# Performance work log

Hardware: AMD Instinct MI355X
Metric: run time of the kernel (lower is better)

## Reference

```python
import jax, jax.numpy as jnp
import numpy as np

DT = 0.01  # RK45 step size ts


def setup_inputs() -> dict:
    key = jax.random.key(0)
    ks = jax.random.split(key, 8)
    B, T, NU, NX, NH, NY = 512, 256, 64, 128, 1024, 16
    scale = 0.05  # keep dynamics stable under explicit integration
    return {
        "u": jax.random.normal(ks[0], (B, T, NU), jnp.float32),
        "x0": jax.random.normal(ks[1], (B, NX), jnp.float32),
        "W1": jax.random.normal(ks[2], (NH, NX + NU), jnp.float32) * scale,
        "b1": jnp.zeros((NH,), jnp.float32),
        "W2": jax.random.normal(ks[3], (NX, NH), jnp.float32) * scale,
        "b2": jnp.zeros((NX,), jnp.float32),
        "C": jax.random.normal(ks[4], (NY, NX), jnp.float32) * scale,
        "D": jax.random.normal(ks[5], (NY, NU), jnp.float32) * scale,
    }


def reference(u, x0, W1, b1, W2, b2, C, D):
    dt = jnp.asarray(DT, u.dtype)

    def ss_model(u_t, x):
        # nonlinear state-space model: dx = W2 tanh(W1 [x;u] + b1) + b2, y = Cx + Du
        z = jnp.concatenate([x, u_t], axis=-1)              # [B, nx+nu]
        k = jnp.tanh(z @ W1.T + b1) @ W2.T + b2             # [B, nx]
        y = x @ C.T + u_t @ D.T                             # [B, ny]
        return k, y

    def step(x, u_t):
        k1, y = ss_model(u_t, x)
        k2, _ = ss_model(u_t, x + dt / 4 * k1)
        k3, _ = ss_model(u_t, x + dt / 32 * (3 * k1 + 9 * k2))
        k4, _ = ss_model(u_t, x + dt / 2197 * (1932 * k1 - 7200 * k2 + 7296 * k3))
        k5, _ = ss_model(u_t, x + dt * (439 * k1 / 216 - 8 * k2 + 3680 * k3 / 513 - 845 * k4 / 4104))
        k6, _ = ss_model(u_t, x + dt * (-8 * k1 / 27 + 2 * k2 - 3544 * k3 / 2565 + 1859 * k4 / 4104 - 11 * k5 / 40))
        dx = dt * (16 * k1 / 135 + 6656 * k3 / 12825 + 28561 * k4 / 56430 - 9 * k5 / 50 + 2 * k6 / 55)
        return x + dx, (x, y)

    u_t_first = jnp.swapaxes(u, 0, 1)                        # [T, B, nu]
    _, (X, Y) = jax.lax.scan(step, x0, u_t_first)
    X_sim = jnp.swapaxes(X, 0, 1)                            # [B, T, nx]
    Y_sim = jnp.swapaxes(Y, 0, 1)                            # [B, T, ny]
    return X_sim, Y_sim
```

## Files before the change

### kernel.cpp

```cpp
#include <hip/hip_runtime.h>

typedef short bf16x8 __attribute__((ext_vector_type(8)));
typedef float f32x4 __attribute__((ext_vector_type(4)));

static constexpr int kT  = 256;
static constexpr int kNU = 64;
static constexpr int kNX = 128;
static constexpr int kNY = 16;
static constexpr int kBT = 16;

static constexpr int kW1P = 64 * 6 * 64 * 8;
static constexpr int kW2P = 8 * 32 * 64 * 8;
static constexpr int kCP  = 4 * 64 * 8;
static constexpr int kDP  = 2 * 64 * 8;
static constexpr int kPackTotal = kW1P + kW2P + kCP + kDP;

__device__ __forceinline__ unsigned short f2bf(float f) {
  union { float f; unsigned int u; } v; v.f = f;
  unsigned int r = v.u + 0x7fffu + ((v.u >> 16) & 1u);
  return (unsigned short)(r >> 16);
}

__global__ __launch_bounds__(256)
void prepack_kernel(const float* __restrict__ W1, const float* __restrict__ W2,
                    const float* __restrict__ C, const float* __restrict__ D,
                    unsigned short* __restrict__ wp) {
  int i = blockIdx.x * 256 + threadIdx.x;
  if (i >= kPackTotal) return;
  float v;
  if (i < kW1P) {
    int j = i & 7, l = (i >> 3) & 63, t = i >> 9;
    int ks = t % 6, n = t / 6;
    v = W1[(16 * n + (l & 15)) * 192 + 32 * ks + 8 * (l >> 4) + j];
  } else if (i < kW1P + kW2P) {
    int k = i - kW1P;
    int j = k & 7, l = (k >> 3) & 63, t = k >> 9;
    int ks = t & 31, n = t >> 5;
    v = W2[(16 * n + (l & 15)) * 1024 + 32 * ks + 8 * (l >> 4) + j];
  } else if (i < kW1P + kW2P + kCP) {
    int k = i - (kW1P + kW2P);
    int j = k & 7, l = (k >> 3) & 63, ks = k >> 9;
    v = C[(l & 15) * 128 + 32 * ks + 8 * (l >> 4) + j];
  } else {
    int k = i - (kW1P + kW2P + kCP);
    int j = k & 7, l = (k >> 3) & 63, ks = k >> 9;
    v = D[(l & 15) * 64 + 32 * ks + 8 * (l >> 4) + j];
  }
  wp[i] = f2bf(v);
}

__constant__ float CTc[5][5] = {
  {(float)(0.01 / 4.0), 0.f, 0.f, 0.f, 0.f},
  {(float)(0.01 * 3.0 / 32.0), (float)(0.01 * 9.0 / 32.0), 0.f, 0.f, 0.f},
  {(float)(0.01 * 1932.0 / 2197.0), (float)(-0.01 * 7200.0 / 2197.0), (float)(0.01 * 7296.0 / 2197.0), 0.f, 0.f},
  {(float)(0.01 * 439.0 / 216.0), (float)(-0.01 * 8.0), (float)(0.01 * 3680.0 / 513.0), (float)(-0.01 * 845.0 / 4104.0), 0.f},
  {(float)(-0.01 * 8.0 / 27.0), (float)(0.01 * 2.0), (float)(-0.01 * 3544.0 / 2565.0), (float)(0.01 * 1859.0 / 4104.0), (float)(-0.01 * 11.0 / 40.0)}
};

__device__ __forceinline__ float tanh_fast(float x) {
  float t = exp2f(x * 2.8853900817779268f);
  return 1.0f - 2.0f * __builtin_amdgcn_rcpf(t + 1.0f);
}

__device__ __forceinline__ void gll16(const void* g, void* l) {
  __builtin_amdgcn_global_load_lds((const __attribute__((address_space(1))) unsigned int*)g,
                                   (__attribute__((address_space(3))) unsigned int*)l, 16, 0, 0);
}

#define MFMA_BF16(A, B, C) __builtin_amdgcn_mfma_f32_16x16x32_bf16(A, B, C, 0, 0, 0)
#define VM_WAIT4 asm volatile("s_waitcnt vmcnt(4)" ::: "memory")
#define BARRIER_LGKM do { asm volatile("s_waitcnt lgkmcnt(0)" ::: "memory"); \
                          __builtin_amdgcn_s_barrier(); } while (0)

#define ISSUE_FRAG(P_) do {                                                    \
    int _p = (P_) & 63;                                                        \
    const char* _src;                                                          \
    if (_p < 32) _src = wpb + (((8 * w + (_p >> 2)) * 6 + (_p & 3)) << 10) + lane * 16; \
    else         _src = wpb + ((size_t)kW1P * 2) + ((w * 32 + (_p - 32)) << 10) + lane * 16; \
    gll16(_src, &wbuf[_p & 7][w][0]);                                          \
  } while (0)

#define READ4(V0_, V1_, V2_, V3_, B_) do {                                     \
    VM_WAIT4;                                                                  \
    V0_ = *(const bf16x8*)&wbuf[((B_) + 0) & 7][w][lane * 8];                  \
    V1_ = *(const bf16x8*)&wbuf[((B_) + 1) & 7][w][lane * 8];                  \
    V2_ = *(const bf16x8*)&wbuf[((B_) + 2) & 7][w][lane * 8];                  \
    V3_ = *(const bf16x8*)&wbuf[((B_) + 3) & 7][w][lane * 8];                  \
  } while (0)

#define REFILL4(B_) do {                                                       \
    __builtin_amdgcn_sched_barrier(0);                                         \
    ISSUE_FRAG((B_) + 8); ISSUE_FRAG((B_) + 9);                                \
    ISSUE_FRAG((B_) + 10); ISSUE_FRAG((B_) + 11);                              \
  } while (0)

__global__ __launch_bounds__(512, 2)
void rk45_kernel(const float* __restrict__ u, const float* __restrict__ x0,
                 const float* __restrict__ b1g, const float* __restrict__ b2g,
                 const unsigned short* __restrict__ wp,
                 float* __restrict__ Xout, float* __restrict__ Yout) {
  __shared__ __align__(16) unsigned short zs[16][232];
  __shared__ __align__(16) unsigned short hs[16][1048];
  __shared__ __align__(16) float xs[16][132];
  __shared__ __align__(16) unsigned short wbuf[8][8][512];

  const int tid  = threadIdx.x;
  const int lane = tid & 63;
  const int w    = tid >> 6;
  const int r16  = lane & 15;
  const int g    = lane >> 4;
  const int b0   = blockIdx.x * kBT;
  const int colw = 16 * w + r16;

  const char* wpb = (const char*)wp;
  const bf16x8* W1P = (const bf16x8*)wp;
  const bf16x8* CP  = (const bf16x8*)(wp + kW1P + kW2P);
  const bf16x8* DP  = (const bf16x8*)(wp + kW1P + kW2P + kCP);

  float b1r[8];
  #pragma unroll
  for (int nt = 0; nt < 8; ++nt)
    b1r[nt] = b1g[128 * w + 16 * nt + r16];
  const float b2reg = b2g[colw];

  float xreg[4];
  f32x4 ubias[8];
  f32x4 k1r = {0,0,0,0}, k2r = {0,0,0,0}, k3r = {0,0,0,0}, k4r = {0,0,0,0}, k5r = {0,0,0,0};

  #pragma unroll
  for (int q = 0; q < 4; ++q) {
    int row = 4 * g + q;
    float xv = x0[(b0 + row) * kNX + colw];
    xreg[q] = xv;
    xs[row][colw] = xv;
    zs[row][colw] = f2bf(xv);
  }

  const int urow = tid >> 5, ucol = (tid & 31) * 2;
  float2 ureg = *(const float2*)&u[((b0 + urow) * kT + 0) * kNU + ucol];

  #pragma unroll
  for (int p = 0; p < 8; ++p) ISSUE_FRAG(p);
  __syncthreads();

  const float D1 = (float)(0.01 * 16.0 / 135.0);
  const float D3 = (float)(0.01 * 6656.0 / 12825.0);
  const float D4 = (float)(0.01 * 28561.0 / 56430.0);
  const float D5 = (float)(-0.01 * 9.0 / 50.0);
  const float D6 = (float)(0.01 * 2.0 / 55.0);

  #pragma unroll 1
  for (int t = 0; t < kT; ++t) {
    {
      int base = tid * 4, row = base >> 7, col = base & 127;
      float4 xv = *(const float4*)&xs[row][col];
      *(float4*)&Xout[((b0 + row) * kT + t) * kNX + col] = xv;
      zs[urow][kNX + ucol]     = f2bf(ureg.x);
      zs[urow][kNX + ucol + 1] = f2bf(ureg.y);
      if (t + 1 < kT)
        ureg = *(const float2*)&u[((b0 + urow) * kT + (t + 1)) * kNU + ucol];
    }
    BARRIER_LGKM;

    {
      bf16x8 zu0 = *(const bf16x8*)&zs[r16][8 * g + 128];
      bf16x8 zu1 = *(const bf16x8*)&zs[r16][8 * g + 160];
      #pragma unroll
      for (int nt = 0; nt < 8; ++nt) {
        int n = 8 * w + nt;
        bf16x8 uw0 = W1P[(n * 6 + 4) * 64 + lane];
        bf16x8 uw1 = W1P[(n * 6 + 5) * 64 + lane];
        float bv = b1r[nt];
        f32x4 ua = {bv, bv, bv, bv};
        ua = MFMA_BF16(zu0, uw0, ua);
        ua = MFMA_BF16(zu1, uw1, ua);
        ubias[nt] = ua;
      }
    }

    #pragma unroll 1
    for (int e = 0; e < 6; ++e) {
      bf16x8 za0 = *(const bf16x8*)&zs[r16][8 * g + 0];
      bf16x8 za1 = *(const bf16x8*)&zs[r16][8 * g + 32];
      bf16x8 za2 = *(const bf16x8*)&zs[r16][8 * g + 64];
      bf16x8 za3 = *(const bf16x8*)&zs[r16][8 * g + 96];

      #pragma unroll
      for (int nt = 0; nt < 8; ++nt) {
        bf16x8 fr0, fr1, fr2, fr3;
        READ4(fr0, fr1, fr2, fr3, 4 * nt);

        f32x4 aa = {0,0,0,0}, ab = {0,0,0,0};
        aa = MFMA_BF16(za0, fr0, aa);
        ab = MFMA_BF16(za1, fr1, ab);
        aa = MFMA_BF16(za2, fr2, aa);
        ab = MFMA_BF16(za3, fr3, ab);
        REFILL4(4 * nt);

        int n = 8 * w + nt;
        #pragma unroll
        for (int q = 0; q < 4; ++q) {
          float hv = tanh_fast(aa[q] + ab[q] + ubias[nt][q]);
          hs[4 * g + q][16 * n + r16] = f2bf(hv);
        }
      }

      if (e == 0 && w == 0) {
        bf16x8 zu0 = *(const bf16x8*)&zs[r16][8 * g + 128];
        bf16x8 zu1 = *(const bf16x8*)&zs[r16][8 * g + 160];
        f32x4 ay = {0,0,0,0};
        ay = MFMA_BF16(za0, CP[0 * 64 + lane], ay);
        ay = MFMA_BF16(za1, CP[1 * 64 + lane], ay);
        ay = MFMA_BF16(za2, CP[2 * 64 + lane], ay);
        ay = MFMA_BF16(za3, CP[3 * 64 + lane], ay);
        ay = MFMA_BF16(zu0, DP[lane], ay);
        ay = MFMA_BF16(zu1, DP[64 + lane], ay);
        #pragma unroll
        for (int q = 0; q < 4; ++q)
          Yout[((b0 + 4 * g + q) * kT + t) * kNY + r16] = ay[q];
      }
      BARRIER_LGKM;

      f32x4 ka = {0,0,0,0}, kb = {0,0,0,0};
      #pragma unroll
      for (int j = 0; j < 8; ++j) {
        bf16x8 g0, g1, g2, g3;
        READ4(g0, g1, g2, g3, 32 + 4 * j);

        bf16x8 h0 = *(const bf16x8*)&hs[r16][8 * g + 32 * (4 * j + 0)];
        bf16x8 h1 = *(const bf16x8*)&hs[r16][8 * g + 32 * (4 * j + 1)];
        bf16x8 h2 = *(const bf16x8*)&hs[r16][8 * g + 32 * (4 * j + 2)];
        bf16x8 h3 = *(const bf16x8*)&hs[r16][8 * g + 32 * (4 * j + 3)];
        ka = MFMA_BF16(h0, g0, ka);
        kb = MFMA_BF16(h1, g1, kb);
        ka = MFMA_BF16(h2, g2, ka);
        kb = MFMA_BF16(h3, g3, kb);
        REFILL4(32 + 4 * j);
      }
      f32x4 kv = ka + kb;
      #pragma unroll
      for (int q = 0; q < 4; ++q) kv[q] += b2reg;

      if      (e == 0) k1r = kv;
      else if (e == 1) k2r = kv;
      else if (e == 2) k3r = kv;
      else if (e == 3) k4r = kv;
      else if (e == 4) k5r = kv;

      if (e < 5) {
        float c1 = CTc[e][0], c2 = CTc[e][1], c3 = CTc[e][2], c4 = CTc[e][3], c5 = CTc[e][4];
        #pragma unroll
        for (int q = 0; q < 4; ++q) {
          float xt = xreg[q] + c1 * k1r[q] + c2 * k2r[q] + c3 * k3r[q] + c4 * k4r[q] + c5 * k5r[q];
          zs[4 * g + q][colw] = f2bf(xt);
        }
      } else {
        #pragma unroll
        for (int q = 0; q < 4; ++q) {
          float xn = xreg[q] + (D1 * k1r[q] + D3 * k3r[q] + D4 * k4r[q] + D5 * k5r[q] + D6 * kv[q]);
          xreg[q] = xn;
          xs[4 * g + q][colw] = xn;
          zs[4 * g + q][colw] = f2bf(xn);
        }
      }
      BARRIER_LGKM;
    }
  }
}

extern "C" void kernel_launch(void* const* d_in, const int* in_sizes, int n_in,
                              void* d_out, int out_size, void* d_ws, size_t ws_size,
                              hipStream_t stream) {
  const float* u  = (const float*)d_in[0];
  const float* x0 = (const float*)d_in[1];
  const float* W1 = (const float*)d_in[2];
  const float* b1 = (const float*)d_in[3];
  const float* W2 = (const float*)d_in[4];
  const float* b2 = (const float*)d_in[5];
  const float* C  = (const float*)d_in[6];
  const float* D  = (const float*)d_in[7];

  unsigned short* wp = (unsigned short*)d_ws;
  float* Xout = (float*)d_out;
  float* Yout = Xout + (size_t)512 * 256 * 128;

  hipLaunchKernelGGL(prepack_kernel, dim3((kPackTotal + 255) / 256), dim3(256), 0, stream,
                     W1, W2, C, D, wp);
  hipLaunchKernelGGL(rk45_kernel, dim3(32), dim3(512), 0, stream,
                     u, x0, b1, b2, (const unsigned short*)wp, Xout, Yout);
}
```

Before: 10.70 ms.

## Stream weight fragments through register ring instead of LDS global_load_lds buffer

Replaces the LDS staging buffer filled by global_load_lds with an 8-entry register ring of bf16x8 fragments. The ring is loaded directly from global memory, with vmcnt waits pacing the prefetch across the W1-u, W1-x and W2 phases. The C/D weights are now staged once in LDS instead of being read from global memory each step, and launch bounds drop to one block per SM so the kernel has room for the extra registers. This removes the LDS round-trip for weights, but relies on manual vmcnt counting being exact. Halving occupancy may also expose global-load latency.

```diff
diff --git a/kernel.cpp b/kernel.cpp
--- a/kernel.cpp
+++ b/kernel.cpp
@@ -62,39 +62,12 @@
   return 1.0f - 2.0f * __builtin_amdgcn_rcpf(t + 1.0f);
 }
 
-__device__ __forceinline__ void gll16(const void* g, void* l) {
-  __builtin_amdgcn_global_load_lds((const __attribute__((address_space(1))) unsigned int*)g,
-                                   (__attribute__((address_space(3))) unsigned int*)l, 16, 0, 0);
-}
-
 #define MFMA_BF16(A, B, C) __builtin_amdgcn_mfma_f32_16x16x32_bf16(A, B, C, 0, 0, 0)
-#define VM_WAIT4 asm volatile("s_waitcnt vmcnt(4)" ::: "memory")
+#define VM_WAIT(N) asm volatile("s_waitcnt vmcnt(" #N ")" ::: "memory")
 #define BARRIER_LGKM do { asm volatile("s_waitcnt lgkmcnt(0)" ::: "memory"); \
                           __builtin_amdgcn_s_barrier(); } while (0)
 
-#define ISSUE_FRAG(P_) do {                                                    \
-    int _p = (P_) & 63;                                                        \
-    const char* _src;                                                          \
-    if (_p < 32) _src = wpb + (((8 * w + (_p >> 2)) * 6 + (_p & 3)) << 10) + lane * 16; \
-    else         _src = wpb + ((size_t)kW1P * 2) + ((w * 32 + (_p - 32)) << 10) + lane * 16; \
-    gll16(_src, &wbuf[_p & 7][w][0]);                                          \
-  } while (0)
-
-#define READ4(V0_, V1_, V2_, V3_, B_) do {                                     \
-    VM_WAIT4;                                                                  \
-    V0_ = *(const bf16x8*)&wbuf[((B_) + 0) & 7][w][lane * 8];                  \
-    V1_ = *(const bf16x8*)&wbuf[((B_) + 1) & 7][w][lane * 8];                  \
-    V2_ = *(const bf16x8*)&wbuf[((B_) + 2) & 7][w][lane * 8];                  \
-    V3_ = *(const bf16x8*)&wbuf[((B_) + 3) & 7][w][lane * 8];                  \
-  } while (0)
-
-#define REFILL4(B_) do {                                                       \
-    __builtin_amdgcn_sched_barrier(0);                                         \
-    ISSUE_FRAG((B_) + 8); ISSUE_FRAG((B_) + 9);                                \
-    ISSUE_FRAG((B_) + 10); ISSUE_FRAG((B_) + 11);                              \
-  } while (0)
-
-__global__ __launch_bounds__(512, 2)
+__global__ __launch_bounds__(512, 1)
 void rk45_kernel(const float* __restrict__ u, const float* __restrict__ x0,
                  const float* __restrict__ b1g, const float* __restrict__ b2g,
                  const unsigned short* __restrict__ wp,
@@ -102,7 +75,7 @@
   __shared__ __align__(16) unsigned short zs[16][232];
   __shared__ __align__(16) unsigned short hs[16][1048];
   __shared__ __align__(16) float xs[16][132];
-  __shared__ __align__(16) unsigned short wbuf[8][8][512];
+  __shared__ __align__(16) unsigned short cdl[384][8];
 
   const int tid  = threadIdx.x;
   const int lane = tid & 63;
@@ -112,10 +85,15 @@
   const int b0   = blockIdx.x * kBT;
   const int colw = 16 * w + r16;
 
-  const char* wpb = (const char*)wp;
   const bf16x8* W1P = (const bf16x8*)wp;
-  const bf16x8* CP  = (const bf16x8*)(wp + kW1P + kW2P);
-  const bf16x8* DP  = (const bf16x8*)(wp + kW1P + kW2P + kCP);
+  const bf16x8* W2P = (const bf16x8*)(wp + kW1P);
+
+#define W1XF(NT, KS) W1P[((8 * w + (NT)) * 6 + (KS)) * 64 + lane]
+#define W1UF(NT, J)  W1P[((8 * w + (NT)) * 6 + 4 + (J)) * 64 + lane]
+#define W2F(IDX)     W2P[(w * 32 + (IDX)) * 64 + lane]
+
+  if (tid < 384)
+    *(bf16x8*)&cdl[tid][0] = ((const bf16x8*)(wp + kW1P + kW2P))[tid];
 
   float b1r[8];
   #pragma unroll
@@ -139,8 +117,10 @@
   const int urow = tid >> 5, ucol = (tid & 31) * 2;
   float2 ureg = *(const float2*)&u[((b0 + urow) * kT + 0) * kNU + ucol];
 
+  bf16x8 ring[8];
   #pragma unroll
-  for (int p = 0; p < 8; ++p) ISSUE_FRAG(p);
+  for (int s = 0; s < 8; ++s)
+    ring[s] = W1UF(s >> 1, s & 1);
   __syncthreads();
 
   const float D1 = (float)(0.01 * 16.0 / 135.0);
@@ -167,9 +147,16 @@
       bf16x8 zu1 = *(const bf16x8*)&zs[r16][8 * g + 160];
       #pragma unroll
       for (int nt = 0; nt < 8; ++nt) {
-        int n = 8 * w + nt;
-        bf16x8 uw0 = W1P[(n * 6 + 4) * 64 + lane];
-        bf16x8 uw1 = W1P[(n * 6 + 5) * 64 + lane];
+        VM_WAIT(6);
+        bf16x8 uw0 = ring[(2 * nt) & 7];
+        bf16x8 uw1 = ring[(2 * nt + 1) & 7];
+        if (nt < 4) {
+          ring[(2 * nt) & 7]     = W1UF(nt + 4, 0);
+          ring[(2 * nt + 1) & 7] = W1UF(nt + 4, 1);
+        } else {
+          ring[(2 * nt) & 7]     = W1XF((2 * nt - 8) >> 2, (2 * nt - 8) & 3);
+          ring[(2 * nt + 1) & 7] = W1XF((2 * nt - 7) >> 2, (2 * nt - 7) & 3);
+        }
         float bv = b1r[nt];
         f32x4 ua = {bv, bv, bv, bv};
         ua = MFMA_BF16(zu0, uw0, ua);
@@ -187,15 +174,23 @@
 
       #pragma unroll
       for (int nt = 0; nt < 8; ++nt) {
-        bf16x8 fr0, fr1, fr2, fr3;
-        READ4(fr0, fr1, fr2, fr3, 4 * nt);
+        VM_WAIT(4);
+        bf16x8 fr0 = ring[(4 * nt + 0) & 7];
+        bf16x8 fr1 = ring[(4 * nt + 1) & 7];
+        bf16x8 fr2 = ring[(4 * nt + 2) & 7];
+        bf16x8 fr3 = ring[(4 * nt + 3) & 7];
+        #pragma unroll
+        for (int r = 0; r < 4; ++r) {
+          const int qr = 4 * nt + 8 + r;
+          if (qr < 32) ring[(4 * nt + r) & 7] = W1XF(qr >> 2, qr & 3);
+          else         ring[(4 * nt + r) & 7] = W2F(qr - 32);
+        }
 
         f32x4 aa = {0,0,0,0}, ab = {0,0,0,0};
         aa = MFMA_BF16(za0, fr0, aa);
         ab = MFMA_BF16(za1, fr1, ab);
         aa = MFMA_BF16(za2, fr2, aa);
         ab = MFMA_BF16(za3, fr3, ab);
-        REFILL4(4 * nt);
 
         int n = 8 * w + nt;
         #pragma unroll
@@ -209,12 +204,12 @@
         bf16x8 zu0 = *(const bf16x8*)&zs[r16][8 * g + 128];
         bf16x8 zu1 = *(const bf16x8*)&zs[r16][8 * g + 160];
         f32x4 ay = {0,0,0,0};
-        ay = MFMA_BF16(za0, CP[0 * 64 + lane], ay);
-        ay = MFMA_BF16(za1, CP[1 * 64 + lane], ay);
-        ay = MFMA_BF16(za2, CP[2 * 64 + lane], ay);
-        ay = MFMA_BF16(za3, CP[3 * 64 + lane], ay);
-        ay = MFMA_BF16(zu0, DP[lane], ay);
-        ay = MFMA_BF16(zu1, DP[64 + lane], ay);
+        ay = MFMA_BF16(za0, *(const bf16x8*)&cdl[0 * 64 + lane][0], ay);
+        ay = MFMA_BF16(za1, *(const bf16x8*)&cdl[1 * 64 + lane][0], ay);
+        ay = MFMA_BF16(za2, *(const bf16x8*)&cdl[2 * 64 + lane][0], ay);
+        ay = MFMA_BF16(za3, *(const bf16x8*)&cdl[3 * 64 + lane][0], ay);
+        ay = MFMA_BF16(zu0, *(const bf16x8*)&cdl[4 * 64 + lane][0], ay);
+        ay = MFMA_BF16(zu1, *(const bf16x8*)&cdl[5 * 64 + lane][0], ay);
         #pragma unroll
         for (int q = 0; q < 4; ++q)
           Yout[((b0 + 4 * g + q) * kT + t) * kNY + r16] = ay[q];
@@ -224,8 +219,18 @@
       f32x4 ka = {0,0,0,0}, kb = {0,0,0,0};
       #pragma unroll
       for (int j = 0; j < 8; ++j) {
-        bf16x8 g0, g1, g2, g3;
-        READ4(g0, g1, g2, g3, 32 + 4 * j);
+        VM_WAIT(4);
+        bf16x8 g0 = ring[(4 * j + 0) & 7];
+        bf16x8 g1 = ring[(4 * j + 1) & 7];
+        bf16x8 g2 = ring[(4 * j + 2) & 7];
+        bf16x8 g3 = ring[(4 * j + 3) & 7];
+        #pragma unroll
+        for (int r = 0; r < 4; ++r) {
+          const int qr = 40 + 4 * j + r;
+          if (qr < 64)    ring[(4 * j + r) & 7] = W2F(qr - 32);
+          else if (e < 5) ring[(4 * j + r) & 7] = W1XF((qr - 64) >> 2, (qr - 64) & 3);
+          else            ring[(4 * j + r) & 7] = W1UF((qr - 64) >> 1, (qr - 64) & 1);
+        }
 
         bf16x8 h0 = *(const bf16x8*)&hs[r16][8 * g + 32 * (4 * j + 0)];
         bf16x8 h1 = *(const bf16x8*)&hs[r16][8 * g + 32 * (4 * j + 1)];
@@ -235,7 +240,6 @@
         kb = MFMA_BF16(h1, g1, kb);
         ka = MFMA_BF16(h2, g2, ka);
         kb = MFMA_BF16(h3, g3, kb);
-        REFILL4(32 + 4 * j);
       }
       f32x4 kv = ka + kb;
       #pragma unroll
```

Result: slower. 11.08 ms (+3.5%).

## Stream weight fragments into registers with pinned first tiles instead of LDS ring

Applied to the files above, without the earlier changes.

Removes the global_load_lds ring buffer in shared memory that streamed W1/W2 fragments. Weights now load straight into registers through two alternating register sets, with each next fragment prefetched right after the current MFMAs. The first W1 and W2 tiles stay resident in registers for the whole run, so each pass refetches fewer fragments. This drops the LDS round trip and the vmcnt waits, but raises register pressure and relies on L1/L2 latency being hidden by one fragment of lookahead.

```diff
diff --git a/kernel.cpp b/kernel.cpp
--- a/kernel.cpp
+++ b/kernel.cpp
@@ -62,39 +62,11 @@
   return 1.0f - 2.0f * __builtin_amdgcn_rcpf(t + 1.0f);
 }
 
-__device__ __forceinline__ void gll16(const void* g, void* l) {
-  __builtin_amdgcn_global_load_lds((const __attribute__((address_space(1))) unsigned int*)g,
-                                   (__attribute__((address_space(3))) unsigned int*)l, 16, 0, 0);
-}
-
 #define MFMA_BF16(A, B, C) __builtin_amdgcn_mfma_f32_16x16x32_bf16(A, B, C, 0, 0, 0)
-#define VM_WAIT4 asm volatile("s_waitcnt vmcnt(4)" ::: "memory")
 #define BARRIER_LGKM do { asm volatile("s_waitcnt lgkmcnt(0)" ::: "memory"); \
                           __builtin_amdgcn_s_barrier(); } while (0)
 
-#define ISSUE_FRAG(P_) do {                                                    \
-    int _p = (P_) & 63;                                                        \
-    const char* _src;                                                          \
-    if (_p < 32) _src = wpb + (((8 * w + (_p >> 2)) * 6 + (_p & 3)) << 10) + lane * 16; \
-    else         _src = wpb + ((size_t)kW1P * 2) + ((w * 32 + (_p - 32)) << 10) + lane * 16; \
-    gll16(_src, &wbuf[_p & 7][w][0]);                                          \
-  } while (0)
-
-#define READ4(V0_, V1_, V2_, V3_, B_) do {                                     \
-    VM_WAIT4;                                                                  \
-    V0_ = *(const bf16x8*)&wbuf[((B_) + 0) & 7][w][lane * 8];                  \
-    V1_ = *(const bf16x8*)&wbuf[((B_) + 1) & 7][w][lane * 8];                  \
-    V2_ = *(const bf16x8*)&wbuf[((B_) + 2) & 7][w][lane * 8];                  \
-    V3_ = *(const bf16x8*)&wbuf[((B_) + 3) & 7][w][lane * 8];                  \
-  } while (0)
-
-#define REFILL4(B_) do {                                                       \
-    __builtin_amdgcn_sched_barrier(0);                                         \
-    ISSUE_FRAG((B_) + 8); ISSUE_FRAG((B_) + 9);                                \
-    ISSUE_FRAG((B_) + 10); ISSUE_FRAG((B_) + 11);                              \
-  } while (0)
-
-__global__ __launch_bounds__(512, 2)
+__global__ __launch_bounds__(512) __attribute__((amdgpu_waves_per_eu(2, 2)))
 void rk45_kernel(const float* __restrict__ u, const float* __restrict__ x0,
                  const float* __restrict__ b1g, const float* __restrict__ b2g,
                  const unsigned short* __restrict__ wp,
@@ -102,7 +74,6 @@
   __shared__ __align__(16) unsigned short zs[16][232];
   __shared__ __align__(16) unsigned short hs[16][1048];
   __shared__ __align__(16) float xs[16][132];
-  __shared__ __align__(16) unsigned short wbuf[8][8][512];
 
   const int tid  = threadIdx.x;
   const int lane = tid & 63;
@@ -112,10 +83,19 @@
   const int b0   = blockIdx.x * kBT;
   const int colw = 16 * w + r16;
 
-  const char* wpb = (const char*)wp;
   const bf16x8* W1P = (const bf16x8*)wp;
+  const bf16x8* W2P = (const bf16x8*)(wp + kW1P);
   const bf16x8* CP  = (const bf16x8*)(wp + kW1P + kW2P);
   const bf16x8* DP  = (const bf16x8*)(wp + kW1P + kW2P + kCP);
+
+#define LOAD_W1X(F0, F1, F2, F3, NT) do {                          \
+    const bf16x8* _p = W1P + (8 * w + (NT)) * 6 * 64 + lane;       \
+    F0 = _p[0]; F1 = _p[64]; F2 = _p[128]; F3 = _p[192];           \
+  } while (0)
+#define LOAD_W2(F0, F1, F2, F3, CC) do {                           \
+    const bf16x8* _p = W2P + (w * 32 + 4 * (CC)) * 64 + lane;      \
+    F0 = _p[0]; F1 = _p[64]; F2 = _p[128]; F3 = _p[192];           \
+  } while (0)
 
   float b1r[8];
   #pragma unroll
@@ -139,8 +119,14 @@
   const int urow = tid >> 5, ucol = (tid & 31) * 2;
   float2 ureg = *(const float2*)&u[((b0 + urow) * kT + 0) * kNU + ucol];
 
-  #pragma unroll
-  for (int p = 0; p < 8; ++p) ISSUE_FRAG(p);
+  bf16x8 p10, p11, p12, p13;
+  bf16x8 p20, p21, p22, p23;
+  bf16x8 fA0, fA1, fA2, fA3;
+  bf16x8 fB0, fB1, fB2, fB3;
+  LOAD_W1X(p10, p11, p12, p13, 0);
+  LOAD_W2 (p20, p21, p22, p23, 0);
+  LOAD_W1X(fA0, fA1, fA2, fA3, 1);
+  LOAD_W1X(fB0, fB1, fB2, fB3, 2);
   __syncthreads();
 
   const float D1 = (float)(0.01 * 16.0 / 135.0);
@@ -185,25 +171,26 @@
       bf16x8 za2 = *(const bf16x8*)&zs[r16][8 * g + 64];
       bf16x8 za3 = *(const bf16x8*)&zs[r16][8 * g + 96];
 
-      #pragma unroll
-      for (int nt = 0; nt < 8; ++nt) {
-        bf16x8 fr0, fr1, fr2, fr3;
-        READ4(fr0, fr1, fr2, fr3, 4 * nt);
-
-        f32x4 aa = {0,0,0,0}, ab = {0,0,0,0};
-        aa = MFMA_BF16(za0, fr0, aa);
-        ab = MFMA_BF16(za1, fr1, ab);
-        aa = MFMA_BF16(za2, fr2, aa);
-        ab = MFMA_BF16(za3, fr3, ab);
-        REFILL4(4 * nt);
-
-        int n = 8 * w + nt;
-        #pragma unroll
-        for (int q = 0; q < 4; ++q) {
-          float hv = tanh_fast(aa[q] + ab[q] + ubias[nt][q]);
-          hs[4 * g + q][16 * n + r16] = f2bf(hv);
-        }
-      }
+#define MM1(NT, F0, F1, F2, F3, ISS)                                   \
+      { f32x4 aa = {0,0,0,0}, ab = {0,0,0,0};                          \
+        aa = MFMA_BF16(za0, F0, aa); ab = MFMA_BF16(za1, F1, ab);      \
+        aa = MFMA_BF16(za2, F2, aa); ab = MFMA_BF16(za3, F3, ab);      \
+        ISS;                                                           \
+        int n = 8 * w + (NT);                                          \
+        _Pragma("unroll")                                              \
+        for (int q = 0; q < 4; ++q) {                                  \
+          float hv = tanh_fast(aa[q] + ab[q] + ubias[NT][q]);          \
+          hs[4 * g + q][16 * n + r16] = f2bf(hv);                      \
+        } }
+      MM1(0, p10, p11, p12, p13, {});
+      MM1(1, fA0, fA1, fA2, fA3, LOAD_W1X(fA0, fA1, fA2, fA3, 3));
+      MM1(2, fB0, fB1, fB2, fB3, LOAD_W1X(fB0, fB1, fB2, fB3, 4));
+      MM1(3, fA0, fA1, fA2, fA3, LOAD_W1X(fA0, fA1, fA2, fA3, 5));
+      MM1(4, fB0, fB1, fB2, fB3, LOAD_W1X(fB0, fB1, fB2, fB3, 6));
+      MM1(5, fA0, fA1, fA2, fA3, LOAD_W1X(fA0, fA1, fA2, fA3, 7));
+      MM1(6, fB0, fB1, fB2, fB3, LOAD_W2(fB0, fB1, fB2, fB3, 1));
+      MM1(7, fA0, fA1, fA2, fA3, LOAD_W2(fA0, fA1, fA2, fA3, 2));
+#undef MM1
 
       if (e == 0 && w == 0) {
         bf16x8 zu0 = *(const bf16x8*)&zs[r16][8 * g + 128];
@@ -222,21 +209,24 @@
       BARRIER_LGKM;
 
       f32x4 ka = {0,0,0,0}, kb = {0,0,0,0};
-      #pragma unroll
-      for (int j = 0; j < 8; ++j) {
-        bf16x8 g0, g1, g2, g3;
-        READ4(g0, g1, g2, g3, 32 + 4 * j);
-
-        bf16x8 h0 = *(const bf16x8*)&hs[r16][8 * g + 32 * (4 * j + 0)];
-        bf16x8 h1 = *(const bf16x8*)&hs[r16][8 * g + 32 * (4 * j + 1)];
-        bf16x8 h2 = *(const bf16x8*)&hs[r16][8 * g + 32 * (4 * j + 2)];
-        bf16x8 h3 = *(const bf16x8*)&hs[r16][8 * g + 32 * (4 * j + 3)];
-        ka = MFMA_BF16(h0, g0, ka);
-        kb = MFMA_BF16(h1, g1, kb);
-        ka = MFMA_BF16(h2, g2, ka);
-        kb = MFMA_BF16(h3, g3, kb);
-        REFILL4(32 + 4 * j);
-      }
+#define MM2(J, F0, F1, F2, F3, ISS)                                          \
+      { bf16x8 h0 = *(const bf16x8*)&hs[r16][8 * g + 32 * (4 * (J) + 0)];    \
+        bf16x8 h1 = *(const bf16x8*)&hs[r16][8 * g + 32 * (4 * (J) + 1)];    \
+        bf16x8 h2 = *(const bf16x8*)&hs[r16][8 * g + 32 * (4 * (J) + 2)];    \
+        bf16x8 h3 = *(const bf16x8*)&hs[r16][8 * g + 32 * (4 * (J) + 3)];    \
+        ka = MFMA_BF16(h0, F0, ka); kb = MFMA_BF16(h1, F1, kb);              \
+        ka = MFMA_BF16(h2, F2, ka); kb = MFMA_BF16(h3, F3, kb);              \
+        ISS; }
+      MM2(0, p20, p21, p22, p23, {});
+      MM2(1, fB0, fB1, fB2, fB3, LOAD_W2(fB0, fB1, fB2, fB3, 3));
+      MM2(2, fA0, fA1, fA2, fA3, LOAD_W2(fA0, fA1, fA2, fA3, 4));
+      MM2(3, fB0, fB1, fB2, fB3, LOAD_W2(fB0, fB1, fB2, fB3, 5));
+      MM2(4, fA0, fA1, fA2, fA3, LOAD_W2(fA0, fA1, fA2, fA3, 6));
+      MM2(5, fB0, fB1, fB2, fB3, LOAD_W2(fB0, fB1, fB2, fB3, 7));
+      MM2(6, fA0, fA1, fA2, fA3, LOAD_W1X(fA0, fA1, fA2, fA3, 1));
+      MM2(7, fB0, fB1, fB2, fB3, LOAD_W1X(fB0, fB1, fB2, fB3, 2));
+#undef MM2
+
       f32x4 kv = ka + kb;
       #pragma unroll
       for (int q = 0; q < 4; ++q) kv[q] += b2reg;
```

Measured after the change: 10.92 ms. +2.1%, slower.
